# Kernel optimization log

Hardware: AMD Instinct MI355X
Metric: run time of the kernel (lower is better)

## Reference

```python
import jax, jax.numpy as jnp
import numpy as np

NEG_SLOPE = 0.2


def _gat_layer(x, edge_index, W, a_src, a_dst, b):
    """PyG GATConv: linear -> per-edge attention logits -> segment softmax over
    destination -> scatter-add weighted messages. Self-loops added (PyG default)."""
    N = x.shape[0]
    heads, out = a_src.shape
    loops = jnp.arange(N, dtype=edge_index.dtype)
    src = jnp.concatenate([edge_index[0], loops])
    dst = jnp.concatenate([edge_index[1], loops])
    xh = (x @ W).reshape(N, heads, out)                      # [N,H,D]
    alpha_s = (xh * a_src).sum(-1)                           # [N,H]
    alpha_d = (xh * a_dst).sum(-1)                           # [N,H]
    e = jax.nn.leaky_relu(alpha_s[src] + alpha_d[dst], NEG_SLOPE)  # [E,H]
    emax = jax.ops.segment_max(e, dst, num_segments=N)       # [N,H]
    ex = jnp.exp(e - emax[dst])
    den = jax.ops.segment_sum(ex, dst, num_segments=N)
    att = ex / (den[dst] + 1e-16)                            # [E,H]
    msg = xh[src] * att[..., None]                           # [E,H,D]
    o = jax.ops.segment_sum(msg, dst, num_segments=N)        # [N,H,D]
    return o.reshape(N, heads * out) + b


def _single_source_gnn(h, edge_index, params):
    n_layers = len(params)
    for i, (W, a_s, a_d, b) in enumerate(params):
        h = _gat_layer(h, edge_index, W, a_s, a_d, b)
        if i < n_layers - 1:
            h = jax.nn.relu(h)
    return h


def setup_inputs() -> dict:
    key = jax.random.key(0)
    B, N, H, heads, deg = 4, 2000, 64, 4, 32
    E = N * deg
    ks = jax.random.split(key, 20)

    def mk_edge_index(k):
        e = jax.random.randint(k, (2, B, E), 0, N)
        off = (jnp.arange(B) * N)[None, :, None]
        return (e + off).reshape(2, B * E).astype(jnp.int32)

    inp = {
        "h0_flat": jax.random.normal(ks[0], (B * N, H), jnp.float32),
        "edge_index_s1": mk_edge_index(ks[1]),
        "edge_index_s2": mk_edge_index(ks[2]),
    }
    dims = [(H, H * heads), (H * heads, H * heads)]
    i = 3
    for s in ("s1", "s2"):
        for l, (din, dout) in enumerate(dims):
            inp[f"W_{s}_{l}"] = jax.random.normal(ks[i], (din, dout), jnp.float32) * 0.1; i += 1
            inp[f"a_src_{s}_{l}"] = jax.random.normal(ks[i], (heads, H), jnp.float32) * 0.1; i += 1
            inp[f"a_dst_{s}_{l}"] = jax.random.normal(ks[i], (heads, H), jnp.float32) * 0.1; i += 1
            inp[f"b_{s}_{l}"] = jnp.zeros((dout,), jnp.float32)
    inp["batch_size"] = B
    inp["num_stocks"] = N
    return inp


def reference(h0_flat, edge_index_s1, edge_index_s2,
              W_s1_0, a_src_s1_0, a_dst_s1_0, b_s1_0,
              W_s1_1, a_src_s1_1, a_dst_s1_1, b_s1_1,
              W_s2_0, a_src_s2_0, a_dst_s2_0, b_s2_0,
              W_s2_1, a_src_s2_1, a_dst_s2_1, b_s2_1,
              batch_size, num_stocks):
    p1 = [(W_s1_0, a_src_s1_0, a_dst_s1_0, b_s1_0),
          (W_s1_1, a_src_s1_1, a_dst_s1_1, b_s1_1)]
    p2 = [(W_s2_0, a_src_s2_0, a_dst_s2_0, b_s2_0),
          (W_s2_1, a_src_s2_1, a_dst_s2_1, b_s2_1)]
    h1 = _single_source_gnn(h0_flat, edge_index_s1, p1)
    h2 = _single_source_gnn(h0_flat, edge_index_s2, p2)
    # dict of per-source outputs in torch -> stacked [n_sources, B*N, H*heads]
    return jnp.stack([h1, h2])
```

## Files before the change

### kernel.cpp

```cpp
#include <hip/hip_runtime.h>
#include <hip/hip_fp16.h>


#define NEG_SLOPE 0.2f
#define ELLW 96

typedef _Float16 half8 __attribute__((ext_vector_type(8)));
typedef float floatx4 __attribute__((ext_vector_type(4)));

struct Args {
    const float* h0;
    const int *ei1, *ei2;
    const float *W10, *W11, *W20, *W21;
    const float *as10, *ad10, *b10, *as11, *ad11, *b11;
    const float *as20, *ad20, *b20, *as21, *ad21, *b21;
    _Float16 *Wt10, *Wt20, *Wt11, *Wt21;
    float *vaS1, *vaD1, *vaS2, *vaD2;
    _Float16 *h0h;
    int *cnt, *slots;
    _Float16 *agg1, *agg2;
    _Float16 *xh1, *xh2;
    float *alS1, *alD1, *alS2, *alD2;
    float *out0, *out1;
    int N, E1, E2, AB;
};


__global__ __launch_bounds__(64) void prep_kernel(Args a) {
    int z = blockIdx.z, y = blockIdx.y, c = blockIdx.x;
    int t = threadIdx.x;
    int flat = ((z * gridDim.y + y) * gridDim.x + c) * 64 + t;
    int GT = gridDim.x * gridDim.y * gridDim.z * 64;
    if (flat < 2 * a.N) a.cnt[flat] = 0;
    for (int i = flat; i < a.N * 64; i += GT)
        a.h0h[i] = (_Float16)a.h0[i];
    if (y == 0) {
        const float* W  = z ? a.W20  : a.W10;
        _Float16*    Wt = z ? a.Wt20 : a.Wt10;
        Wt[(size_t)c * 64 + t] = (_Float16)W[(size_t)t * 256 + c];
        if (c < 8) {
            int h = c & 3, sel = c >> 2;
            const float* av = sel ? (z ? a.ad20 : a.ad10)
                                  : (z ? a.as20 : a.as10);
            float* va = sel ? (z ? a.vaD2 : a.vaD1)
                            : (z ? a.vaS2 : a.vaS1);
            float acc = 0.f;
            for (int cc = 0; cc < 64; cc++)
                acc += W[(size_t)t * 256 + h * 64 + cc] * av[h * 64 + cc];
            va[h * 64 + t] = acc;
        }
    } else {
        int k = (y - 1) * 64 + t;
        const float* W  = z ? a.W21  : a.W11;
        _Float16*    Wt = z ? a.Wt21 : a.Wt11;
        Wt[(size_t)c * 256 + k] = (_Float16)W[(size_t)k * 256 + c];
    }
}


__global__ __launch_bounds__(256) void scat_al0_kernel(Args a) {
    int b = blockIdx.x;
    int tid = threadIdx.x;
    if (b < a.AB) {
        int g = b * 4 + (tid >> 6);
        if (g >= 2 * a.N) return;
        int L = tid & 63;
        int s = (g >= a.N) ? 1 : 0;
        int i = g - s * a.N;
        const float* vaS = s ? a.vaS2 : a.vaS1;
        const float* vaD = s ? a.vaD2 : a.vaD1;
        float* alS = s ? a.alS2 : a.alS1;
        float* alD = s ? a.alD2 : a.alD1;
        float x = a.h0[(size_t)i * 64 + L];
#pragma unroll
        for (int h = 0; h < 4; h++) {
            float sv = x * vaS[h * 64 + L];
            float dv = x * vaD[h * 64 + L];
#pragma unroll
            for (int off = 32; off >= 1; off >>= 1) {
                sv += __shfl_xor(sv, off);
                dv += __shfl_xor(dv, off);
            }
            if (L == 0) {
                alS[i * 4 + h] = sv;
                alD[i * 4 + h] = dv;
            }
        }
    } else {
        int i = (b - a.AB) * 256 + tid;
        int tot1 = a.E1 + a.N, tot2 = a.E2 + a.N;
        if (i >= tot1 + tot2) return;
        int s, j; const int* ei; int E;
        if (i < tot1) { s = 0; j = i;        ei = a.ei1; E = a.E1; }
        else          { s = 1; j = i - tot1; ei = a.ei2; E = a.E2; }
        int src, dst;
        if (j < E) { src = ei[j]; dst = ei[E + j]; }
        else       { src = dst = j - E; }
        int gg = s * a.N + dst;
        int pos = atomicAdd(&a.cnt[gg], 1);
        if (pos < ELLW) a.slots[(size_t)gg * ELLW + pos] = src;
    }
}


__global__ __launch_bounds__(256) void attn_agg_kernel(Args a) {
    __shared__ float2 pairs[4][8][10];
    int tid = threadIdx.x;
    int h = tid >> 6, L = tid & 63, st = L >> 3, lc = L & 7;
    int b = blockIdx.x;
    int cpx = (2 * a.N) >> 3;
    int g = (b & 7) * cpx + (b >> 3);
    int s = (g >= a.N) ? 1 : 0;
    int dst = g - s * a.N;
    const float* alS = s ? a.alS2 : a.alS1;
    const float* alD = s ? a.alD2 : a.alD1;
    _Float16*    agg = s ? a.agg2 : a.agg1;

    const int* slots = a.slots + (size_t)g * ELLW;
    int pre = slots[L];
    int nd = a.cnt[g];
    if (nd > ELLW) nd = ELLW;
    float ad = alD[dst * 4 + h];
    const char* xb = (const char*)a.h0h + lc * 16;

    float acc[8] = {};
    float pden = 0.f;

    for (int c = 0; c < nd; c += 64) {
        int n = nd - c; if (n > 64) n = 64;
        int off = 0; float p = 0.f;
        if (L < n) {
            int src = (c == 0) ? pre : slots[c + L];
            float t = alS[src * 4 + h] + ad;
            t = (t > 0.f) ? t : NEG_SLOPE * t;
            p = __expf(t);
            off = src * 128;
        }
        pden += p;
        pairs[h][L & 7][L >> 3] = make_float2(__int_as_float(off), p);
        int iters = (n + 7) >> 3;
        for (int ii = 0; ii < iters; ii += 4) {
            float4 twoA = *(const float4*)&pairs[h][st][ii];
            float4 twoB = *(const float4*)&pairs[h][st][ii + 2];
            int   o0 = __float_as_int(twoA.x); float w0 = twoA.y;
            int   o1i = __float_as_int(twoA.z); float w1 = twoA.w;
            int   o2i = __float_as_int(twoB.x); float w2 = twoB.y;
            int   o3i = __float_as_int(twoB.z); float w3 = twoB.w;
            float4 r0 = *(const float4*)(xb + o0);
            float4 r1 = *(const float4*)(xb + o1i);
            float4 r2 = *(const float4*)(xb + o2i);
            float4 r3 = *(const float4*)(xb + o3i);
            const __half2* q0 = (const __half2*)&r0;
            const __half2* q1 = (const __half2*)&r1;
            const __half2* q2 = (const __half2*)&r2;
            const __half2* q3 = (const __half2*)&r3;
#pragma unroll
            for (int k = 0; k < 4; k++) {
                acc[2 * k + 0] += (float)q0[k].x * w0;
                acc[2 * k + 1] += (float)q0[k].y * w0;
                acc[2 * k + 0] += (float)q1[k].x * w1;
                acc[2 * k + 1] += (float)q1[k].y * w1;
                acc[2 * k + 0] += (float)q2[k].x * w2;
                acc[2 * k + 1] += (float)q2[k].y * w2;
                acc[2 * k + 0] += (float)q3[k].x * w3;
                acc[2 * k + 1] += (float)q3[k].y * w3;
            }
        }
    }
#pragma unroll
    for (int k = 0; k < 8; k++) {
        acc[k] += __shfl_xor(acc[k], 8);
        acc[k] += __shfl_xor(acc[k], 16);
        acc[k] += __shfl_xor(acc[k], 32);
    }
#pragma unroll
    for (int o2_ = 32; o2_ >= 1; o2_ >>= 1) pden += __shfl_xor(pden, o2_);

    if (st == 0) {
        float d = 1.0f / (pden + 1e-16f);
        int col = h * 64 + lc * 8;
        half8 ov;
#pragma unroll
        for (int k = 0; k < 8; k++) ov[k] = (_Float16)(acc[k] * d);
        *(half8*)(agg + (size_t)dst * 256 + col) = ov;
    }
}


__global__ __launch_bounds__(256) void fusedgemm_kernel(Args a) {
    __shared__ _Float16 hT[32][264];
    int half_ = (a.N / 32);
    int b = blockIdx.x;
    int s = (b >= half_);
    int bx = b - s * half_;
    int row0 = bx * 32;

    const _Float16* agg = s ? a.agg2 : a.agg1;
    const _Float16* Wt0 = s ? a.Wt20 : a.Wt10;
    const _Float16* Wt1 = s ? a.Wt21 : a.Wt11;
    const float* bias0  = s ? a.b20  : a.b10;
    const float* a_s    = s ? a.as21 : a.as11;
    const float* a_d    = s ? a.ad21 : a.ad11;
    _Float16* xh = s ? a.xh2 : a.xh1;
    float* alS = s ? a.alS2 : a.alS1;
    float* alD = s ? a.alD2 : a.alD1;

    int tid  = threadIdx.x;
    int wave = tid >> 6;
    int lane = tid & 63;
    int lo = lane & 15, hi = lane >> 4;
    int c0 = wave * 64;

    {
        floatx4 acc[2][4] = {};
#pragma unroll
        for (int ks = 0; ks < 2; ks++) {
            half8 af[2], bf[4];
#pragma unroll
            for (int f = 0; f < 2; f++)
                af[f] = *(const half8*)(agg + (size_t)(row0 + f * 16 + lo) * 256
                                        + c0 + ks * 32 + hi * 8);
#pragma unroll
            for (int cf = 0; cf < 4; cf++)
                bf[cf] = *(const half8*)(Wt0 + (size_t)(c0 + cf * 16 + lo) * 64
                                         + ks * 32 + hi * 8);
#pragma unroll
            for (int f = 0; f < 2; f++)
#pragma unroll
                for (int cf = 0; cf < 4; cf++)
                    acc[f][cf] = __builtin_amdgcn_mfma_f32_16x16x32_f16(
                        af[f], bf[cf], acc[f][cf], 0, 0, 0);
        }
        float bb[4];
#pragma unroll
        for (int cf = 0; cf < 4; cf++) bb[cf] = bias0[c0 + cf * 16 + lo];
#pragma unroll
        for (int f = 0; f < 2; f++)
#pragma unroll
            for (int cf = 0; cf < 4; cf++)
#pragma unroll
                for (int r = 0; r < 4; r++) {
                    int row = f * 16 + hi * 4 + r;
                    float v = acc[f][cf][r] + bb[cf];
                    hT[row][c0 + cf * 16 + lo] = (_Float16)fmaxf(v, 0.f);
                }
    }
    __syncthreads();

    floatx4 acc[2][4] = {};
#pragma unroll
    for (int ks = 0; ks < 8; ks++) {
        half8 af[2], bf[4];
#pragma unroll
        for (int f = 0; f < 2; f++)
            af[f] = *(const half8*)&hT[f * 16 + lo][ks * 32 + hi * 8];
#pragma unroll
        for (int cf = 0; cf < 4; cf++)
            bf[cf] = *(const half8*)(Wt1 + (size_t)(c0 + cf * 16 + lo) * 256
                                     + ks * 32 + hi * 8);
#pragma unroll
        for (int f = 0; f < 2; f++)
#pragma unroll
            for (int cf = 0; cf < 4; cf++)
                acc[f][cf] = __builtin_amdgcn_mfma_f32_16x16x32_f16(
                    af[f], bf[cf], acc[f][cf], 0, 0, 0);
    }

    float asw[4], adw[4];
#pragma unroll
    for (int cf = 0; cf < 4; cf++) {
        asw[cf] = a_s[c0 + cf * 16 + lo];
        adw[cf] = a_d[c0 + cf * 16 + lo];
    }
#pragma unroll
    for (int f = 0; f < 2; f++) {
#pragma unroll
        for (int r = 0; r < 4; r++) {
            int row = row0 + f * 16 + hi * 4 + r;
            float v0 = acc[f][0][r], v1 = acc[f][1][r];
            float v2 = acc[f][2][r], v3 = acc[f][3][r];
            _Float16* xrow = &xh[(size_t)row * 256 + c0 + lo];
            xrow[0]  = (_Float16)v0;
            xrow[16] = (_Float16)v1;
            xrow[32] = (_Float16)v2;
            xrow[48] = (_Float16)v3;
            float s1 = v0 * asw[0] + v1 * asw[1] + v2 * asw[2] + v3 * asw[3];
            float s2 = v0 * adw[0] + v1 * adw[1] + v2 * adw[2] + v3 * adw[3];
#pragma unroll
            for (int off = 1; off < 16; off <<= 1) {
                s1 += __shfl_xor(s1, off);
                s2 += __shfl_xor(s2, off);
            }
            if (lo == 0) {
                alS[row * 4 + wave] = s1;
                alD[row * 4 + wave] = s2;
            }
        }
    }
}


__global__ __launch_bounds__(256) void attn1_kernel(Args a) {
    __shared__ float2 pairs[4][8][10];
    int tid = threadIdx.x;
    int h = tid >> 6, L = tid & 63, st = L >> 3, lc = L & 7;
    int b = blockIdx.x;
    int cpx = (2 * a.N) >> 3;
    int g = (b & 7) * cpx + (b >> 3);
    int s = (g >= a.N) ? 1 : 0;
    int dst = g - s * a.N;
    const _Float16* xh = s ? a.xh2  : a.xh1;
    const float* alS   = s ? a.alS2 : a.alS1;
    const float* alD   = s ? a.alD2 : a.alD1;
    const float* bias  = s ? a.b21  : a.b11;
    float* out         = s ? a.out1 : a.out0;

    const int* slots = a.slots + (size_t)g * ELLW;
    int pre = slots[L];
    int nd = a.cnt[g];
    if (nd > ELLW) nd = ELLW;
    float ad = alD[dst * 4 + h];
    const char* xb = (const char*)xh + h * 128 + lc * 16;

    float acc[8] = {};
    float pden = 0.f;

    for (int c = 0; c < nd; c += 64) {
        int n = nd - c; if (n > 64) n = 64;
        int off = 0; float p = 0.f;
        if (L < n) {
            int src = (c == 0) ? pre : slots[c + L];
            float t = alS[src * 4 + h] + ad;
            t = (t > 0.f) ? t : NEG_SLOPE * t;
            p = __expf(t);
            off = src * 512;
        }
        pden += p;
        pairs[h][L & 7][L >> 3] = make_float2(__int_as_float(off), p);
        int iters = (n + 7) >> 3;
        for (int ii = 0; ii < iters; ii += 4) {
            float4 twoA = *(const float4*)&pairs[h][st][ii];
            float4 twoB = *(const float4*)&pairs[h][st][ii + 2];
            int   o0 = __float_as_int(twoA.x); float w0 = twoA.y;
            int   o1i = __float_as_int(twoA.z); float w1 = twoA.w;
            int   o2i = __float_as_int(twoB.x); float w2 = twoB.y;
            int   o3i = __float_as_int(twoB.z); float w3 = twoB.w;
            float4 r0 = *(const float4*)(xb + o0);
            float4 r1 = *(const float4*)(xb + o1i);
            float4 r2 = *(const float4*)(xb + o2i);
            float4 r3 = *(const float4*)(xb + o3i);
            const __half2* q0 = (const __half2*)&r0;
            const __half2* q1 = (const __half2*)&r1;
            const __half2* q2 = (const __half2*)&r2;
            const __half2* q3 = (const __half2*)&r3;
#pragma unroll
            for (int k = 0; k < 4; k++) {
                acc[2 * k + 0] += (float)q0[k].x * w0;
                acc[2 * k + 1] += (float)q0[k].y * w0;
                acc[2 * k + 0] += (float)q1[k].x * w1;
                acc[2 * k + 1] += (float)q1[k].y * w1;
                acc[2 * k + 0] += (float)q2[k].x * w2;
                acc[2 * k + 1] += (float)q2[k].y * w2;
                acc[2 * k + 0] += (float)q3[k].x * w3;
                acc[2 * k + 1] += (float)q3[k].y * w3;
            }
        }
    }
#pragma unroll
    for (int k = 0; k < 8; k++) {
        acc[k] += __shfl_xor(acc[k], 8);
        acc[k] += __shfl_xor(acc[k], 16);
        acc[k] += __shfl_xor(acc[k], 32);
    }
#pragma unroll
    for (int o2_ = 32; o2_ >= 1; o2_ >>= 1) pden += __shfl_xor(pden, o2_);

    if (st == 0) {
        float d = 1.0f / (pden + 1e-16f);
        int col = h * 64 + lc * 8;
        float4 bA = *(const float4*)&bias[col];
        float4 bB = *(const float4*)&bias[col + 4];
        float4 oA, oB;
        oA.x = acc[0] * d + bA.x; oA.y = acc[1] * d + bA.y;
        oA.z = acc[2] * d + bA.z; oA.w = acc[3] * d + bA.w;
        oB.x = acc[4] * d + bB.x; oB.y = acc[5] * d + bB.y;
        oB.z = acc[6] * d + bB.z; oB.w = acc[7] * d + bB.w;
        *(float4*)&out[(size_t)dst * 256 + col] = oA;
        *(float4*)&out[(size_t)dst * 256 + col + 4] = oB;
    }
}


extern "C" void kernel_launch(void* const* d_in, const int* in_sizes, int n_in,
                              void* d_out, int out_size, void* d_ws, size_t ws_size,
                              hipStream_t stream) {
    const int N  = in_sizes[0] / 64;
    const int E1 = in_sizes[1] / 2;
    const int E2 = in_sizes[2] / 2;

    char* base = (char*)d_ws;
    size_t off = 0;
    auto carve = [&](size_t bytes) -> void* {
        void* p = base + off;
        off += (bytes + 255) & ~(size_t)255;
        return p;
    };
    int* cnt        = (int*)carve((size_t)2 * N * 4);
    int* slots      = (int*)carve((size_t)2 * N * ELLW * 4);
    _Float16* agg1  = (_Float16*)carve((size_t)N * 256 * 2);
    _Float16* agg2  = (_Float16*)carve((size_t)N * 256 * 2);
    _Float16* xh1   = (_Float16*)carve((size_t)N * 256 * 2);
    _Float16* xh2   = (_Float16*)carve((size_t)N * 256 * 2);
    float* alS1     = (float*)carve((size_t)N * 4 * 4);
    float* alD1     = (float*)carve((size_t)N * 4 * 4);
    float* alS2     = (float*)carve((size_t)N * 4 * 4);
    float* alD2     = (float*)carve((size_t)N * 4 * 4);
    _Float16* Wt10  = (_Float16*)carve((size_t)256 * 64 * 2);
    _Float16* Wt20  = (_Float16*)carve((size_t)256 * 64 * 2);
    _Float16* Wt11  = (_Float16*)carve((size_t)256 * 256 * 2);
    _Float16* Wt21  = (_Float16*)carve((size_t)256 * 256 * 2);
    float* vaS1     = (float*)carve((size_t)256 * 4);
    float* vaD1     = (float*)carve((size_t)256 * 4);
    float* vaS2     = (float*)carve((size_t)256 * 4);
    float* vaD2     = (float*)carve((size_t)256 * 4);
    _Float16* h0h   = (_Float16*)carve((size_t)N * 64 * 2);
    (void)ws_size; (void)n_in;

    Args a;
    a.h0 = (const float*)d_in[0];
    a.ei1 = (const int*)d_in[1];
    a.ei2 = (const int*)d_in[2];
    a.W10 = (const float*)d_in[3];  a.as10 = (const float*)d_in[4];
    a.ad10 = (const float*)d_in[5]; a.b10 = (const float*)d_in[6];
    a.W11 = (const float*)d_in[7];  a.as11 = (const float*)d_in[8];
    a.ad11 = (const float*)d_in[9]; a.b11 = (const float*)d_in[10];
    a.W20 = (const float*)d_in[11]; a.as20 = (const float*)d_in[12];
    a.ad20 = (const float*)d_in[13]; a.b20 = (const float*)d_in[14];
    a.W21 = (const float*)d_in[15]; a.as21 = (const float*)d_in[16];
    a.ad21 = (const float*)d_in[17]; a.b21 = (const float*)d_in[18];
    a.Wt10 = Wt10; a.Wt20 = Wt20; a.Wt11 = Wt11; a.Wt21 = Wt21;
    a.vaS1 = vaS1; a.vaD1 = vaD1; a.vaS2 = vaS2; a.vaD2 = vaD2;
    a.h0h = h0h;
    a.cnt = cnt; a.slots = slots;
    a.agg1 = agg1; a.agg2 = agg2;
    a.xh1 = xh1; a.xh2 = xh2;
    a.alS1 = alS1; a.alD1 = alD1; a.alS2 = alS2; a.alD2 = alD2;
    a.out0 = (float*)d_out; a.out1 = (float*)d_out + (size_t)N * 256;
    a.N = N; a.E1 = E1; a.E2 = E2;
    a.AB = (2 * N + 3) / 4;

    int tot = (E1 + N) + (E2 + N);
    int scatterBlocks = (tot + 255) / 256;

    prep_kernel<<<dim3(256, 5, 2), 64, 0, stream>>>(a);
    scat_al0_kernel<<<a.AB + scatterBlocks, 256, 0, stream>>>(a);
    attn_agg_kernel<<<2 * N, 256, 0, stream>>>(a);
    fusedgemm_kernel<<<(N / 32) * 2, 256, 0, stream>>>(a);
    attn1_kernel<<<2 * N, 256, 0, stream>>>(a);
}
```

Measured before the change: 120.1 us.

## Partition edge scatter by destination range matching XCD block mapping

The edge-to-ELL scatter now launches eight blocks per edge chunk, one per destination range matching the (b&7) XCD interleave used by the aggregation kernel. Each block reads every edge's dst and performs the atomic and slot write only for destinations in its range. The aim is to keep each counter's atomics and slot writes within one XCD's L2, avoiding cross-die coherence traffic and sharing that L2 locality with the later aggregation. The cost is that dst indices are read eight times, along with extra filtering work.

```diff
diff --git a/kernel.cpp b/kernel.cpp
--- a/kernel.cpp
+++ b/kernel.cpp
@@ -4,6 +4,7 @@
 
 #define NEG_SLOPE 0.2f
 #define ELLW 96
+#define EPT 8
 
 typedef _Float16 half8 __attribute__((ext_vector_type(8)));
 typedef float floatx4 __attribute__((ext_vector_type(4)));
@@ -87,18 +88,28 @@
             }
         }
     } else {
-        int i = (b - a.AB) * 256 + tid;
-        int tot1 = a.E1 + a.N, tot2 = a.E2 + a.N;
-        if (i >= tot1 + tot2) return;
-        int s, j; const int* ei; int E;
-        if (i < tot1) { s = 0; j = i;        ei = a.ei1; E = a.E1; }
-        else          { s = 1; j = i - tot1; ei = a.ei2; E = a.E2; }
-        int src, dst;
-        if (j < E) { src = ei[j]; dst = ei[E + j]; }
-        else       { src = dst = j - E; }
-        int gg = s * a.N + dst;
-        int pos = atomicAdd(&a.cnt[gg], 1);
-        if (pos < ELLW) a.slots[(size_t)gg * ELLW + pos] = src;
+        int sb = b - a.AB;
+        int r = sb & 7;
+        int chunk = sb >> 3;
+        int cpx = (2 * a.N) >> 3;
+        int glo = r * cpx, ghi = glo + cpx;
+        int tot1 = a.E1 + a.N;
+        int tot = tot1 + a.E2 + a.N;
+        int base = chunk * (256 * EPT);
+#pragma unroll
+        for (int k = 0; k < EPT; k++) {
+            int j = base + k * 256 + tid;
+            if (j >= tot) break;
+            int s, jj; const int* ei; int E;
+            if (j < tot1) { s = 0; jj = j;        ei = a.ei1; E = a.E1; }
+            else          { s = 1; jj = j - tot1; ei = a.ei2; E = a.E2; }
+            int dst = (jj < E) ? ei[E + jj] : (jj - E);
+            int gg = s * a.N + dst;
+            if (gg < glo || gg >= ghi) continue;
+            int src = (jj < E) ? ei[jj] : dst;
+            int pos = atomicAdd(&a.cnt[gg], 1);
+            if (pos < ELLW) a.slots[(size_t)gg * ELLW + pos] = src;
+        }
     }
 }
 
@@ -450,7 +461,8 @@
     a.AB = (2 * N + 3) / 4;
 
     int tot = (E1 + N) + (E2 + N);
-    int scatterBlocks = (tot + 255) / 256;
+    int chunks = (tot + 256 * EPT - 1) / (256 * EPT);
+    int scatterBlocks = chunks * 8;
 
     prep_kernel<<<dim3(256, 5, 2), 64, 0, stream>>>(a);
     scat_al0_kernel<<<a.AB + scatterBlocks, 256, 0, stream>>>(a);
```

New measurement: 114.1 us. 1.05x faster.
